# Kernel optimization log

Hardware: AMD Instinct MI355X
Metric: run time of the kernel (lower is better)

Reference implementation:

```python
import jax, jax.numpy as jnp
import numpy as np

HIDDEN = 2048
NH = 32          # num attention heads
NKV = 8          # num key/value heads
HD = HIDDEN // NH  # head_dim = 64
ROPE_BASE = 10000.0
NEG_INF = -1e9


def _rope_interleaved(t, positions):
    # t: [b, s, h, d], interleaved RoPE over full head_dim (flash-attn RotaryEmbedding(interleaved=True))
    d = t.shape[-1]
    inv_freq = 1.0 / (ROPE_BASE ** (jnp.arange(0, d, 2, dtype=jnp.float32) / d))
    ang = positions[:, None].astype(jnp.float32) * inv_freq[None, :]  # [s, d/2]
    cos = jnp.cos(ang)[None, :, None, :]
    sin = jnp.sin(ang)[None, :, None, :]
    t1 = t[..., 0::2]
    t2 = t[..., 1::2]
    out_even = t1 * cos - t2 * sin
    out_odd = t1 * sin + t2 * cos
    return jnp.stack([out_even, out_odd], axis=-1).reshape(t.shape)


def setup_inputs() -> dict:
    key = jax.random.key(0)
    k1, k2, k3 = jax.random.split(key, 3)
    B, S = 2, 2048
    x = jax.random.normal(k1, (B, S, HIDDEN), dtype=jnp.float32)
    mask = jnp.ones((B, S), dtype=jnp.int32)  # padding mask, all valid
    total_head_dim = (NH + 2 * NKV) * HD  # 3072
    scale = 1.0 / np.sqrt(HIDDEN)
    w_qkv = jax.random.normal(k2, (HIDDEN, total_head_dim), dtype=jnp.float32) * scale
    w_o = jax.random.normal(k3, (NH * HD, HIDDEN), dtype=jnp.float32) * scale
    return {"x": x, "mask": mask, "w_qkv": w_qkv, "w_o": w_o}


def reference(x, mask, w_qkv, w_o):
    B, S, _ = x.shape
    kv_size = NKV * HD
    qkv = jnp.einsum('bsh,hd->bsd', x, w_qkv)
    q = qkv[..., :HIDDEN].reshape(B, S, NH, HD)
    kv = qkv[..., HIDDEN:].reshape(B, S, 2, NKV, HD)
    pos = jnp.arange(S)  # seqlen_offset = 0 (input_pos None)
    q = _rope_interleaved(q, pos)
    k = _rope_interleaved(kv[:, :, 0], pos)
    v = kv[:, :, 1]
    # GQA: expand kv heads to NH
    groups = NH // NKV
    k = jnp.repeat(k, groups, axis=2)  # [b, s, NH, HD]
    v = jnp.repeat(v, groups, axis=2)
    scores = jnp.einsum('bqhd,bkhd->bhqk', q, k) / np.sqrt(HD)
    causal = jnp.tril(jnp.ones((S, S), dtype=bool))
    key_valid = mask[:, None, None, :] > 0  # [b,1,1,k]
    scores = jnp.where(causal[None, None] & key_valid, scores, NEG_INF)
    probs = jax.nn.softmax(scores, axis=-1)
    attn = jnp.einsum('bhqk,bkhd->bqhd', probs, v)
    # pad_input writes zeros at padded query positions
    attn = attn * (mask[:, :, None, None] > 0)
    attn = attn.reshape(B, S, NH * HD)
    return jnp.einsum('bsd,dh->bsh', attn, w_o)
```

## Files before the change

kernel.cpp:

```cpp
#include <hip/hip_runtime.h>
#include <hip/hip_bf16.h>
#include <cstdint>
#include <cstddef>

typedef __attribute__((ext_vector_type(8))) short bf16x8;
typedef __attribute__((ext_vector_type(4))) float f32x4;

static constexpr int CB  = 2;
static constexpr int CS  = 2048;
static constexpr int CH  = 2048;
static constexpr int CNH = 32;
static constexpr int CNKV = 8;
static constexpr int CHD = 64;
static constexpr int CTHD = 3072;

__device__ __forceinline__ void gload_lds16(const void* g, void* l) {
  __builtin_amdgcn_global_load_lds(
      (const __attribute__((address_space(1))) unsigned int*)g,
      (__attribute__((address_space(3))) unsigned int*)l, 16, 0, 0);
}

__device__ __forceinline__ unsigned short bfbits(float f) {
  __hip_bfloat16 h = __float2bfloat16(f);
  return *(unsigned short*)&h;
}

__global__ void conv_bf16(const float* __restrict__ in, __hip_bfloat16* __restrict__ out, int n) {
  const int i = (blockIdx.x * 256 + threadIdx.x) * 4;
  if (i >= n) return;
  const float4 v = *(const float4*)(in + i);
  out[i]     = __float2bfloat16(v.x);
  out[i + 1] = __float2bfloat16(v.y);
  out[i + 2] = __float2bfloat16(v.z);
  out[i + 3] = __float2bfloat16(v.w);
}

__global__ __launch_bounds__(256) void transpose_conv(const float* __restrict__ in,
                                                      __hip_bfloat16* __restrict__ out,
                                                      int R, int Cc) {
  __shared__ float t[32][33];
  const int nbx = Cc >> 5;
  const int bx = blockIdx.x % nbx, by = blockIdx.x / nbx;
  const int c0 = bx << 5, r0 = by << 5;
  const int tx = threadIdx.x & 31, ty = threadIdx.x >> 5;
#pragma unroll
  for (int j = 0; j < 32; j += 8)
    t[ty + j][tx] = in[(size_t)(r0 + ty + j) * Cc + c0 + tx];
  __syncthreads();
#pragma unroll
  for (int j = 0; j < 32; j += 8)
    out[(size_t)(c0 + ty + j) * R + r0 + tx] = __float2bfloat16(t[tx][ty + j]);
}

template <typename OutT>
__global__ __launch_bounds__(256) void gemm_bt(const __hip_bfloat16* __restrict__ A,
                                               const __hip_bfloat16* __restrict__ Bt,
                                               OutT* __restrict__ C, int M, int N, int K) {
  __shared__ __hip_bfloat16 As[128 * 32];
  __shared__ __hip_bfloat16 Bs[128 * 32];
  const int tid = threadIdx.x;
  const int lane = tid & 63;
  const int wave = tid >> 6;
  const int nTn = N >> 7;
  const int nwg = gridDim.x;
  const int wg = (blockIdx.x & 7) * (nwg >> 3) + (blockIdx.x >> 3);
  const int tm = wg / nTn, tn = wg % nTn;
  const size_t m0 = (size_t)tm * 128, n0 = (size_t)tn * 128;
  const __hip_bfloat16* Ag = A + m0 * K;
  const __hip_bfloat16* Bg = Bt + n0 * K;
  const int wr = wave >> 1, wc = wave & 1;
  const int rsel = lane & 15, k8 = (lane >> 4) << 3;

  f32x4 acc[4][4];
#pragma unroll
  for (int m = 0; m < 4; ++m)
#pragma unroll
    for (int n = 0; n < 4; ++n) acc[m][n] = (f32x4){0.f, 0.f, 0.f, 0.f};

  for (int k0 = 0; k0 < K; k0 += 32) {
    __syncthreads();
#pragma unroll
    for (int i = 0; i < 2; ++i) {
      const int c = i * 256 + tid;
      const int r = c >> 2, kq = (c & 3) << 3;
      gload_lds16(Ag + (size_t)r * K + k0 + kq, &As[(i * 256 + wave * 64) * 8]);
      gload_lds16(Bg + (size_t)r * K + k0 + kq, &Bs[(i * 256 + wave * 64) * 8]);
    }
    __syncthreads();
    bf16x8 af[4], bfr[4];
#pragma unroll
    for (int m = 0; m < 4; ++m)
      af[m] = *(const bf16x8*)&As[(wr * 64 + m * 16 + rsel) * 32 + k8];
#pragma unroll
    for (int n = 0; n < 4; ++n)
      bfr[n] = *(const bf16x8*)&Bs[(wc * 64 + n * 16 + rsel) * 32 + k8];
#pragma unroll
    for (int m = 0; m < 4; ++m)
#pragma unroll
      for (int n = 0; n < 4; ++n)
        acc[m][n] = __builtin_amdgcn_mfma_f32_16x16x32_bf16(af[m], bfr[n], acc[m][n], 0, 0, 0);
  }

  const int rowb = (lane >> 4) << 2;
#pragma unroll
  for (int m = 0; m < 4; ++m)
#pragma unroll
    for (int n = 0; n < 4; ++n) {
      const size_t r0 = m0 + wr * 64 + m * 16 + rowb;
      const size_t cc = n0 + wc * 64 + n * 16 + rsel;
#pragma unroll
      for (int j = 0; j < 4; ++j) {
        const float v = acc[m][n][j];
        if constexpr (sizeof(OutT) == 4)
          C[(r0 + j) * N + cc] = v;
        else
          C[(r0 + j) * N + cc] = __float2bfloat16(v);
      }
    }
}

__global__ void rope_extract(const __hip_bfloat16* __restrict__ qkv,
                             __hip_bfloat16* __restrict__ Q,
                             __hip_bfloat16* __restrict__ Kr) {
  const int idx = blockIdx.x * 256 + threadIdx.x;
  const int i = idx & 31;
  const int hs = (idx >> 5) % 40;
  const int r = idx / (40 * 32);
  const int srow = r & (CS - 1);
  const int b = r >> 11;
  const float inv = exp2f(-(float)i * (13.287712379549449f / 32.0f));
  const float ang = (float)srow * inv;
  const float sn = sinf(ang), cs = cosf(ang);
  const int col = (hs < CNH) ? hs * CHD + 2 * i : CH + (hs - CNH) * CHD + 2 * i;
  const float t1 = __bfloat162float(qkv[(size_t)r * CTHD + col]);
  const float t2 = __bfloat162float(qkv[(size_t)r * CTHD + col + 1]);
  const float scl = (hs < CNH) ? 0.18033688011112042f : 1.0f;
  const float ev = (t1 * cs - t2 * sn) * scl;
  const float ov = (t1 * sn + t2 * cs) * scl;
  __hip_bfloat16* dst;
  if (hs < CNH)
    dst = Q + ((((size_t)b * CNH + hs) * CS + srow) * CHD + 2 * i);
  else
    dst = Kr + ((((size_t)b * CNKV + (hs - CNH)) * CS + srow) * CHD + 2 * i);
  dst[0] = __float2bfloat16(ev);
  dst[1] = __float2bfloat16(ov);
}

__global__ __launch_bounds__(256) void v_transpose(const __hip_bfloat16* __restrict__ qkv,
                                                   __hip_bfloat16* __restrict__ VT) {
  __shared__ __hip_bfloat16 t[64][72];
  const int bi = blockIdx.x;
  const int stile = bi & 31;
  const int kvh = (bi >> 5) & 7;
  const int b = bi >> 8;
  const int tx = threadIdx.x & 63;
  const int ty = threadIdx.x >> 6;
  const int s0 = stile * 64;
#pragma unroll
  for (int j = 0; j < 16; ++j) {
    const int sl = ty * 16 + j;
    t[sl][tx] = qkv[(size_t)(b * CS + s0 + sl) * CTHD + (CH + CNKV * CHD) + kvh * CHD + tx];
  }
  __syncthreads();
#pragma unroll
  for (int j = 0; j < 16; ++j) {
    const int dl = ty * 16 + j;
    VT[(((size_t)b * CNKV + kvh) * CHD + dl) * CS + s0 + tx] = t[tx][dl];
  }
}

__global__ __launch_bounds__(256) void attn_fa(const __hip_bfloat16* __restrict__ Q,
                                               const __hip_bfloat16* __restrict__ Kr,
                                               const __hip_bfloat16* __restrict__ VT,
                                               const int* __restrict__ mask,
                                               __hip_bfloat16* __restrict__ O) {
  __shared__ __hip_bfloat16 Ks[2][64 * 64];
  __shared__ __hip_bfloat16 Vs[2][64 * 64];
  __shared__ __hip_bfloat16 P4[4][16][72];
  const int kvh = blockIdx.x & 7;
  const int slot = blockIdx.x >> 3;
  const int qw = 127 - (slot >> 1);
  const int b = slot & 1;
  const int tid = threadIdx.x;
  const int wave = tid >> 6, lane = tid & 63;
  const int h = kvh * 4 + wave;
  const int q0 = qw * 16;
  const int rsel = lane & 15;
  const int hi = lane >> 4;
  const int k8 = hi * 8;
  const int rowb = hi * 4;
  const int qr = q0 + rsel;
  const __hip_bfloat16* Qp = Q + (((size_t)b * CNH + h) * CS + q0) * CHD;
  const __hip_bfloat16* Kp = Kr + ((size_t)b * CNKV + kvh) * CS * CHD;
  const __hip_bfloat16* Vp = VT + ((size_t)b * CNKV + kvh) * CHD * CS;
  const int* mp = mask + b * CS;
  __hip_bfloat16(*P)[72] = P4[wave];

  bf16x8 qf[2];
  qf[0] = *(const bf16x8*)(Qp + rsel * CHD + k8);
  qf[1] = *(const bf16x8*)(Qp + rsel * CHD + 32 + k8);

  f32x4 o[4];
#pragma unroll
  for (int nt = 0; nt < 4; ++nt) o[nt] = (f32x4){0.f, 0.f, 0.f, 0.f};
  float mrun = -3e38f, lrun = 0.f;

  const int nkb = (qw >> 2) + 1;

  auto stage = [&](int buf, int key0) {
#pragma unroll
    for (int half = 0; half < 2; ++half) {
      const int c = half * 256 + tid;
      const int r = c >> 3;
      const int swz = ((c & 7) ^ (r & 7)) * 8;
      __hip_bfloat16* kd = &Ks[buf][(half * 256 + wave * 64) * 8];
      __hip_bfloat16* vd = &Vs[buf][(half * 256 + wave * 64) * 8];
      gload_lds16(Kp + (size_t)(key0 + r) * CHD + swz, kd);
      gload_lds16(Vp + (size_t)r * CS + key0 + swz, vd);
    }
  };

  int mcur = mp[lane], mnext = 0;
  stage(0, 0);
  __syncthreads();

  for (int t = 0; t < nkb; ++t) {
    const int cur = t & 1;
    const int key0 = t * 64;
    const bool last = (t == nkb - 1);
    if (!last) {
      stage(cur ^ 1, key0 + 64);
      mnext = mp[key0 + 64 + lane];
    }
    const unsigned long long kvbits = __ballot(mcur > 0);
    const int sz = rsel & 7;
    bf16x8 kc[8];
#pragma unroll
    for (int kt = 0; kt < 4; ++kt) {
      const int row = (kt * 16 + rsel) * 64;
      kc[kt * 2]     = *(const bf16x8*)&Ks[cur][row + ((hi ^ sz) << 3)];
      kc[kt * 2 + 1] = *(const bf16x8*)&Ks[cur][row + (((hi ^ 4) ^ sz) << 3)];
    }
    f32x4 st[4];
#pragma unroll
    for (int kt = 0; kt < 4; ++kt) {
      f32x4 s = (f32x4){0.f, 0.f, 0.f, 0.f};
      s = __builtin_amdgcn_mfma_f32_16x16x32_bf16(kc[kt * 2], qf[0], s, 0, 0, 0);
      s = __builtin_amdgcn_mfma_f32_16x16x32_bf16(kc[kt * 2 + 1], qf[1], s, 0, 0, 0);
      st[kt] = s;
    }
    bf16x8 vf[8];
#pragma unroll
    for (int nt = 0; nt < 4; ++nt) {
      const int row = (nt * 16 + rsel) * 64;
      vf[nt * 2]     = *(const bf16x8*)&Vs[cur][row + ((hi ^ sz) << 3)];
      vf[nt * 2 + 1] = *(const bf16x8*)&Vs[cur][row + (((hi ^ 4) ^ sz) << 3)];
    }
    if (!(kvbits == ~0ull && !last)) {
#pragma unroll
      for (int kt = 0; kt < 4; ++kt)
#pragma unroll
        for (int j = 0; j < 4; ++j) {
          const int idx = kt * 16 + rowb + j;
          const bool bad = !((kvbits >> idx) & 1ull) || (last && key0 + idx > qr);
          if (bad) st[kt][j] = -1e9f;
        }
    }
    float pmax = st[0][0];
#pragma unroll
    for (int kt = 0; kt < 4; ++kt)
#pragma unroll
      for (int j = 0; j < 4; ++j) pmax = fmaxf(pmax, st[kt][j]);
    pmax = fmaxf(pmax, __shfl_xor(pmax, 16));
    pmax = fmaxf(pmax, __shfl_xor(pmax, 32));
    if (__any(pmax > mrun + 8.0f)) {
      const float mn = fmaxf(mrun, pmax);
      const float al = exp2f(mrun - mn);
      mrun = mn;
      lrun *= al;
#pragma unroll
      for (int nt = 0; nt < 4; ++nt)
#pragma unroll
        for (int j = 0; j < 4; ++j) o[nt][j] *= al;
    }
    float ps = 0.f;
#pragma unroll
    for (int kt = 0; kt < 4; ++kt)
#pragma unroll
      for (int j = 0; j < 4; ++j) {
        const float p = exp2f(st[kt][j] - mrun);
        st[kt][j] = p;
        ps += p;
      }
    ps += __shfl_xor(ps, 16);
    ps += __shfl_xor(ps, 32);
    lrun += ps;
#pragma unroll
    for (int kt = 0; kt < 4; ++kt) {
      ushort4 pk;
      pk.x = bfbits(st[kt][0]);
      pk.y = bfbits(st[kt][1]);
      pk.z = bfbits(st[kt][2]);
      pk.w = bfbits(st[kt][3]);
      *(ushort4*)&P[rsel][kt * 16 + rowb] = pk;
    }
    const bf16x8 pb0 = *(const bf16x8*)&P[rsel][k8];
    const bf16x8 pb1 = *(const bf16x8*)&P[rsel][32 + k8];
#pragma unroll
    for (int nt = 0; nt < 4; ++nt) {
      o[nt] = __builtin_amdgcn_mfma_f32_16x16x32_bf16(vf[nt * 2], pb0, o[nt], 0, 0, 0);
      o[nt] = __builtin_amdgcn_mfma_f32_16x16x32_bf16(vf[nt * 2 + 1], pb1, o[nt], 0, 0, 0);
    }
    __syncthreads();
    mcur = mnext;
  }

  const float qm = (mp[qr] > 0) ? 1.0f : 0.0f;
  const float inv = qm / fmaxf(lrun, 1e-20f);
  __hip_bfloat16* Orow = O + (((size_t)b * CS + qr) * CNH + h) * CHD;
#pragma unroll
  for (int nt = 0; nt < 4; ++nt) {
    ushort4 ok;
    ok.x = bfbits(o[nt][0] * inv);
    ok.y = bfbits(o[nt][1] * inv);
    ok.z = bfbits(o[nt][2] * inv);
    ok.w = bfbits(o[nt][3] * inv);
    *(ushort4*)(Orow + nt * 16 + rowb) = ok;
  }
}

extern "C" void kernel_launch(void* const* d_in, const int* in_sizes, int n_in,
                              void* d_out, int out_size, void* d_ws, size_t ws_size,
                              hipStream_t stream) {
  const float* x = (const float*)d_in[0];
  const int* mask = (const int*)d_in[1];
  const float* w_qkv = (const float*)d_in[2];
  const float* w_o = (const float*)d_in[3];
  float* out = (float*)d_out;

  char* ws = (char*)d_ws;
  size_t off = 0;
  auto alloc = [&](size_t bytes) {
    char* p = ws + off;
    off += (bytes + 255) & ~(size_t)255;
    return p;
  };
  const size_t M = (size_t)CB * CS;
  __hip_bfloat16* x_bf  = (__hip_bfloat16*)alloc(M * CH * 2);
  __hip_bfloat16* wqkvT = (__hip_bfloat16*)alloc((size_t)CTHD * CH * 2);
  __hip_bfloat16* woT   = (__hip_bfloat16*)alloc((size_t)CH * CH * 2);
  __hip_bfloat16* qkv   = (__hip_bfloat16*)alloc(M * CTHD * 2);
  __hip_bfloat16* Qb    = (__hip_bfloat16*)alloc((size_t)CB * CNH * CS * CHD * 2);
  __hip_bfloat16* Kb    = (__hip_bfloat16*)alloc((size_t)CB * CNKV * CS * CHD * 2);
  __hip_bfloat16* VTb   = (__hip_bfloat16*)alloc((size_t)CB * CNKV * CHD * CS * 2);
  __hip_bfloat16* attnb = (__hip_bfloat16*)alloc(M * CH * 2);

  conv_bf16<<<(int)(M * CH / 4 / 256), 256, 0, stream>>>(x, x_bf, (int)(M * CH));
  transpose_conv<<<(CTHD / 32) * (CH / 32), 256, 0, stream>>>(w_qkv, wqkvT, CH, CTHD);
  transpose_conv<<<(CH / 32) * (CH / 32), 256, 0, stream>>>(w_o, woT, CH, CH);
  gemm_bt<__hip_bfloat16><<<(int)(M / 128) * (CTHD / 128), 256, 0, stream>>>(
      x_bf, wqkvT, qkv, (int)M, CTHD, CH);
  rope_extract<<<(int)(M * 40 * 32 / 256), 256, 0, stream>>>(qkv, Qb, Kb);
  v_transpose<<<CB * CNKV * 32, 256, 0, stream>>>(qkv, VTb);
  attn_fa<<<CB * CNKV * 128, 256, 0, stream>>>(Qb, Kb, VTb, mask, attnb);
  gemm_bt<float><<<(int)(M / 128) * (CH / 128), 256, 0, stream>>>(
      attnb, woT, out, (int)M, CH, CH);
}
```

Baseline: 247.0 us.

## Process two 16-row query sub-tiles per wave in flash attention

```diff
diff --git a/kernel.cpp b/kernel.cpp
--- a/kernel.cpp
+++ b/kernel.cpp
@@ -176,36 +176,39 @@
                                                __hip_bfloat16* __restrict__ O) {
   __shared__ __hip_bfloat16 Ks[2][64 * 64];
   __shared__ __hip_bfloat16 Vs[2][64 * 64];
-  __shared__ __hip_bfloat16 P4[4][16][72];
+  __shared__ __hip_bfloat16 P4[4][2][16][72];
   const int kvh = blockIdx.x & 7;
   const int slot = blockIdx.x >> 3;
-  const int qw = 127 - (slot >> 1);
+  const int qw = 63 - (slot >> 1);
   const int b = slot & 1;
   const int tid = threadIdx.x;
   const int wave = tid >> 6, lane = tid & 63;
   const int h = kvh * 4 + wave;
-  const int q0 = qw * 16;
+  const int q0 = qw * 32;
   const int rsel = lane & 15;
   const int hi = lane >> 4;
   const int k8 = hi * 8;
   const int rowb = hi * 4;
-  const int qr = q0 + rsel;
   const __hip_bfloat16* Qp = Q + (((size_t)b * CNH + h) * CS + q0) * CHD;
   const __hip_bfloat16* Kp = Kr + ((size_t)b * CNKV + kvh) * CS * CHD;
   const __hip_bfloat16* Vp = VT + ((size_t)b * CNKV + kvh) * CHD * CS;
   const int* mp = mask + b * CS;
-  __hip_bfloat16(*P)[72] = P4[wave];
-
-  bf16x8 qf[2];
-  qf[0] = *(const bf16x8*)(Qp + rsel * CHD + k8);
-  qf[1] = *(const bf16x8*)(Qp + rsel * CHD + 32 + k8);
-
-  f32x4 o[4];
-#pragma unroll
-  for (int nt = 0; nt < 4; ++nt) o[nt] = (f32x4){0.f, 0.f, 0.f, 0.f};
-  float mrun = -3e38f, lrun = 0.f;
-
-  const int nkb = (qw >> 2) + 1;
+
+  bf16x8 qf[2][2];
+#pragma unroll
+  for (int s = 0; s < 2; ++s) {
+    qf[s][0] = *(const bf16x8*)(Qp + (s * 16 + rsel) * CHD + k8);
+    qf[s][1] = *(const bf16x8*)(Qp + (s * 16 + rsel) * CHD + 32 + k8);
+  }
+
+  f32x4 o[2][4];
+#pragma unroll
+  for (int s = 0; s < 2; ++s)
+#pragma unroll
+    for (int nt = 0; nt < 4; ++nt) o[s][nt] = (f32x4){0.f, 0.f, 0.f, 0.f};
+  float mrun[2] = {-3e38f, -3e38f}, lrun[2] = {0.f, 0.f};
+
+  const int nkb = (qw >> 1) + 1;
 
   auto stage = [&](int buf, int key0) {
 #pragma unroll
@@ -241,14 +244,75 @@
       kc[kt * 2]     = *(const bf16x8*)&Ks[cur][row + ((hi ^ sz) << 3)];
       kc[kt * 2 + 1] = *(const bf16x8*)&Ks[cur][row + (((hi ^ 4) ^ sz) << 3)];
     }
-    f32x4 st[4];
+    f32x4 st[2][4];
 #pragma unroll
     for (int kt = 0; kt < 4; ++kt) {
-      f32x4 s = (f32x4){0.f, 0.f, 0.f, 0.f};
-      s = __builtin_amdgcn_mfma_f32_16x16x32_bf16(kc[kt * 2], qf[0], s, 0, 0, 0);
-      s = __builtin_amdgcn_mfma_f32_16x16x32_bf16(kc[kt * 2 + 1], qf[1], s, 0, 0, 0);
-      st[kt] = s;
-    }
+#pragma unroll
+      for (int s = 0; s < 2; ++s) {
+        f32x4 acc = (f32x4){0.f, 0.f, 0.f, 0.f};
+        acc = __builtin_amdgcn_mfma_f32_16x16x32_bf16(kc[kt * 2], qf[s][0], acc, 0, 0, 0);
+        acc = __builtin_amdgcn_mfma_f32_16x16x32_bf16(kc[kt * 2 + 1], qf[s][1], acc, 0, 0, 0);
+        st[s][kt] = acc;
+      }
+    }
+#pragma unroll
+    for (int s = 0; s < 2; ++s) {
+      const int qs = q0 + s * 16;
+      const int qr = qs + rsel;
+      if (kvbits != ~0ull || key0 + 63 > qs) {
+#pragma unroll
+        for (int kt = 0; kt < 4; ++kt)
+#pragma unroll
+          for (int j = 0; j < 4; ++j) {
+            const int idx = kt * 16 + rowb + j;
+            const bool bad = !((kvbits >> idx) & 1ull) || (key0 + idx > qr);
+            if (bad) st[s][kt][j] = -1e9f;
+          }
+      }
+    }
+#pragma unroll
+    for (int s = 0; s < 2; ++s) {
+      float pmax = st[s][0][0];
+#pragma unroll
+      for (int kt = 0; kt < 4; ++kt)
+#pragma unroll
+        for (int j = 0; j < 4; ++j) pmax = fmaxf(pmax, st[s][kt][j]);
+      pmax = fmaxf(pmax, __shfl_xor(pmax, 16));
+      pmax = fmaxf(pmax, __shfl_xor(pmax, 32));
+      if (__any(pmax > mrun[s] + 8.0f)) {
+        const float mn = fmaxf(mrun[s], pmax);
+        const float al = exp2f(mrun[s] - mn);
+        mrun[s] = mn;
+        lrun[s] *= al;
+#pragma unroll
+        for (int nt = 0; nt < 4; ++nt)
+#pragma unroll
+          for (int j = 0; j < 4; ++j) o[s][nt][j] *= al;
+      }
+      float ps = 0.f;
+#pragma unroll
+      for (int kt = 0; kt < 4; ++kt)
+#pragma unroll
+        for (int j = 0; j < 4; ++j) {
+          const float p = exp2f(st[s][kt][j] - mrun[s]);
+          st[s][kt][j] = p;
+          ps += p;
+        }
+      ps += __shfl_xor(ps, 16);
+      ps += __shfl_xor(ps, 32);
+      lrun[s] += ps;
+    }
+#pragma unroll
+    for (int s = 0; s < 2; ++s)
+#pragma unroll
+      for (int kt = 0; kt < 4; ++kt) {
+        ushort4 pk;
+        pk.x = bfbits(st[s][kt][0]);
+        pk.y = bfbits(st[s][kt][1]);
+        pk.z = bfbits(st[s][kt][2]);
+        pk.w = bfbits(st[s][kt][3]);
+        *(ushort4*)&P4[wave][s][rsel][kt * 16 + rowb] = pk;
+      }
     bf16x8 vf[8];
 #pragma unroll
     for (int nt = 0; nt < 4; ++nt) {
@@ -256,76 +320,38 @@
       vf[nt * 2]     = *(const bf16x8*)&Vs[cur][row + ((hi ^ sz) << 3)];
       vf[nt * 2 + 1] = *(const bf16x8*)&Vs[cur][row + (((hi ^ 4) ^ sz) << 3)];
     }
-    if (!(kvbits == ~0ull && !last)) {
-#pragma unroll
-      for (int kt = 0; kt < 4; ++kt)
-#pragma unroll
-        for (int j = 0; j < 4; ++j) {
-          const int idx = kt * 16 + rowb + j;
-          const bool bad = !((kvbits >> idx) & 1ull) || (last && key0 + idx > qr);
-          if (bad) st[kt][j] = -1e9f;
-        }
-    }
-    float pmax = st[0][0];
-#pragma unroll
-    for (int kt = 0; kt < 4; ++kt)
-#pragma unroll
-      for (int j = 0; j < 4; ++j) pmax = fmaxf(pmax, st[kt][j]);
-    pmax = fmaxf(pmax, __shfl_xor(pmax, 16));
-    pmax = fmaxf(pmax, __shfl_xor(pmax, 32));
-    if (__any(pmax > mrun + 8.0f)) {
-      const float mn = fmaxf(mrun, pmax);
-      const float al = exp2f(mrun - mn);
-      mrun = mn;
-      lrun *= al;
-#pragma unroll
-      for (int nt = 0; nt < 4; ++nt)
-#pragma unroll
-        for (int j = 0; j < 4; ++j) o[nt][j] *= al;
-    }
-    float ps = 0.f;
-#pragma unroll
-    for (int kt = 0; kt < 4; ++kt)
-#pragma unroll
-      for (int j = 0; j < 4; ++j) {
-        const float p = exp2f(st[kt][j] - mrun);
-        st[kt][j] = p;
-        ps += p;
-      }
-    ps += __shfl_xor(ps, 16);
-    ps += __shfl_xor(ps, 32);
-    lrun += ps;
-#pragma unroll
-    for (int kt = 0; kt < 4; ++kt) {
-      ushort4 pk;
-      pk.x = bfbits(st[kt][0]);
-      pk.y = bfbits(st[kt][1]);
-      pk.z = bfbits(st[kt][2]);
-      pk.w = bfbits(st[kt][3]);
-      *(ushort4*)&P[rsel][kt * 16 + rowb] = pk;
-    }
-    const bf16x8 pb0 = *(const bf16x8*)&P[rsel][k8];
-    const bf16x8 pb1 = *(const bf16x8*)&P[rsel][32 + k8];
-#pragma unroll
-    for (int nt = 0; nt < 4; ++nt) {
-      o[nt] = __builtin_amdgcn_mfma_f32_16x16x32_bf16(vf[nt * 2], pb0, o[nt], 0, 0, 0);
-      o[nt] = __builtin_amdgcn_mfma_f32_16x16x32_bf16(vf[nt * 2 + 1], pb1, o[nt], 0, 0, 0);
-    }
+    bf16x8 pb[2][2];
+#pragma unroll
+    for (int s = 0; s < 2; ++s) {
+      pb[s][0] = *(const bf16x8*)&P4[wave][s][rsel][k8];
+      pb[s][1] = *(const bf16x8*)&P4[wave][s][rsel][32 + k8];
+    }
+#pragma unroll
+    for (int nt = 0; nt < 4; ++nt)
+#pragma unroll
+      for (int s = 0; s < 2; ++s) {
+        o[s][nt] = __builtin_amdgcn_mfma_f32_16x16x32_bf16(vf[nt * 2], pb[s][0], o[s][nt], 0, 0, 0);
+        o[s][nt] = __builtin_amdgcn_mfma_f32_16x16x32_bf16(vf[nt * 2 + 1], pb[s][1], o[s][nt], 0, 0, 0);
+      }
     __syncthreads();
     mcur = mnext;
   }
 
-  const float qm = (mp[qr] > 0) ? 1.0f : 0.0f;
-  const float inv = qm / fmaxf(lrun, 1e-20f);
-  __hip_bfloat16* Orow = O + (((size_t)b * CS + qr) * CNH + h) * CHD;
-#pragma unroll
-  for (int nt = 0; nt < 4; ++nt) {
-    ushort4 ok;
-    ok.x = bfbits(o[nt][0] * inv);
-    ok.y = bfbits(o[nt][1] * inv);
-    ok.z = bfbits(o[nt][2] * inv);
-    ok.w = bfbits(o[nt][3] * inv);
-    *(ushort4*)(Orow + nt * 16 + rowb) = ok;
+#pragma unroll
+  for (int s = 0; s < 2; ++s) {
+    const int qr = q0 + s * 16 + rsel;
+    const float qm = (mp[qr] > 0) ? 1.0f : 0.0f;
+    const float inv = qm / fmaxf(lrun[s], 1e-20f);
+    __hip_bfloat16* Orow = O + (((size_t)b * CS + qr) * CNH + h) * CHD;
+#pragma unroll
+    for (int nt = 0; nt < 4; ++nt) {
+      ushort4 ok;
+      ok.x = bfbits(o[s][nt][0] * inv);
+      ok.y = bfbits(o[s][nt][1] * inv);
+      ok.z = bfbits(o[s][nt][2] * inv);
+      ok.w = bfbits(o[s][nt][3] * inv);
+      *(ushort4*)(Orow + nt * 16 + rowb) = ok;
+    }
   }
 }
 
@@ -362,7 +388,7 @@
       x_bf, wqkvT, qkv, (int)M, CTHD, CH);
   rope_extract<<<(int)(M * 40 * 32 / 256), 256, 0, stream>>>(qkv, Qb, Kb);
   v_transpose<<<CB * CNKV * 32, 256, 0, stream>>>(qkv, VTb);
-  attn_fa<<<CB * CNKV * 128, 256, 0, stream>>>(Qb, Kb, VTb, mask, attnb);
+  attn_fa<<<CB * CNKV * 64, 256, 0, stream>>>(Qb, Kb, VTb, mask, attnb);
   gemm_bt<float><<<(int)(M / 128) * (CH / 128), 256, 0, stream>>>(
       attnb, woT, out, (int)M, CH, CH);
 }
```

New measurement: 293.3 us. +18.7%, slower.

## Fuse RoPE, Q/K scatter and V transpose into QKV GEMM epilogue

Applied to the files above, without the earlier changes.

```diff
diff --git a/kernel.cpp b/kernel.cpp
--- a/kernel.cpp
+++ b/kernel.cpp
@@ -33,6 +33,14 @@
   out[i + 1] = __float2bfloat16(v.y);
   out[i + 2] = __float2bfloat16(v.z);
   out[i + 3] = __float2bfloat16(v.w);
+}
+
+__global__ void trig_table(float2* __restrict__ tab) {
+  const int idx = blockIdx.x * 256 + threadIdx.x;
+  const int s = idx >> 5, i = idx & 31;
+  const float inv = exp2f(-(float)i * (13.287712379549449f / 32.0f));
+  const float ang = (float)s * inv;
+  tab[idx] = make_float2(cosf(ang), sinf(ang));
 }
 
 __global__ __launch_bounds__(256) void transpose_conv(const float* __restrict__ in,
@@ -119,54 +127,105 @@
     }
 }
 
-__global__ void rope_extract(const __hip_bfloat16* __restrict__ qkv,
-                             __hip_bfloat16* __restrict__ Q,
-                             __hip_bfloat16* __restrict__ Kr) {
-  const int idx = blockIdx.x * 256 + threadIdx.x;
-  const int i = idx & 31;
-  const int hs = (idx >> 5) % 40;
-  const int r = idx / (40 * 32);
-  const int srow = r & (CS - 1);
-  const int b = r >> 11;
-  const float inv = exp2f(-(float)i * (13.287712379549449f / 32.0f));
-  const float ang = (float)srow * inv;
-  const float sn = sinf(ang), cs = cosf(ang);
-  const int col = (hs < CNH) ? hs * CHD + 2 * i : CH + (hs - CNH) * CHD + 2 * i;
-  const float t1 = __bfloat162float(qkv[(size_t)r * CTHD + col]);
-  const float t2 = __bfloat162float(qkv[(size_t)r * CTHD + col + 1]);
-  const float scl = (hs < CNH) ? 0.18033688011112042f : 1.0f;
-  const float ev = (t1 * cs - t2 * sn) * scl;
-  const float ov = (t1 * sn + t2 * cs) * scl;
-  __hip_bfloat16* dst;
-  if (hs < CNH)
-    dst = Q + ((((size_t)b * CNH + hs) * CS + srow) * CHD + 2 * i);
-  else
-    dst = Kr + ((((size_t)b * CNKV + (hs - CNH)) * CS + srow) * CHD + 2 * i);
-  dst[0] = __float2bfloat16(ev);
-  dst[1] = __float2bfloat16(ov);
-}
-
-__global__ __launch_bounds__(256) void v_transpose(const __hip_bfloat16* __restrict__ qkv,
-                                                   __hip_bfloat16* __restrict__ VT) {
-  __shared__ __hip_bfloat16 t[64][72];
-  const int bi = blockIdx.x;
-  const int stile = bi & 31;
-  const int kvh = (bi >> 5) & 7;
-  const int b = bi >> 8;
-  const int tx = threadIdx.x & 63;
-  const int ty = threadIdx.x >> 6;
-  const int s0 = stile * 64;
-#pragma unroll
-  for (int j = 0; j < 16; ++j) {
-    const int sl = ty * 16 + j;
-    t[sl][tx] = qkv[(size_t)(b * CS + s0 + sl) * CTHD + (CH + CNKV * CHD) + kvh * CHD + tx];
+__global__ __launch_bounds__(256) void gemm_qkv(const __hip_bfloat16* __restrict__ A,
+                                                const __hip_bfloat16* __restrict__ Bt,
+                                                const float2* __restrict__ tab,
+                                                __hip_bfloat16* __restrict__ Qb,
+                                                __hip_bfloat16* __restrict__ Kb,
+                                                __hip_bfloat16* __restrict__ VTb) {
+  constexpr int M = CB * CS, N = CTHD, K = CH;
+  __shared__ __hip_bfloat16 As[128 * 32];
+  __shared__ __hip_bfloat16 Bs[128 * 32];
+  const int tid = threadIdx.x;
+  const int lane = tid & 63;
+  const int wave = tid >> 6;
+  const int nTn = N >> 7;
+  const int nwg = gridDim.x;
+  const int wg = (blockIdx.x & 7) * (nwg >> 3) + (blockIdx.x >> 3);
+  const int tm = wg / nTn, tn = wg % nTn;
+  const int m0 = tm * 128, n0 = tn * 128;
+  const __hip_bfloat16* Ag = A + (size_t)m0 * K;
+  const __hip_bfloat16* Bg = Bt + (size_t)n0 * K;
+  const int wr = wave >> 1, wc = wave & 1;
+  const int rsel = lane & 15, k8 = (lane >> 4) << 3;
+
+  f32x4 acc[4][4];
+#pragma unroll
+  for (int m = 0; m < 4; ++m)
+#pragma unroll
+    for (int n = 0; n < 4; ++n) acc[m][n] = (f32x4){0.f, 0.f, 0.f, 0.f};
+
+  for (int k0 = 0; k0 < K; k0 += 32) {
+    __syncthreads();
+#pragma unroll
+    for (int i = 0; i < 2; ++i) {
+      const int c = i * 256 + tid;
+      const int r = c >> 2, kq = (c & 3) << 3;
+      gload_lds16(Ag + (size_t)r * K + k0 + kq, &As[(i * 256 + wave * 64) * 8]);
+      gload_lds16(Bg + (size_t)r * K + k0 + kq, &Bs[(i * 256 + wave * 64) * 8]);
+    }
+    __syncthreads();
+    bf16x8 af[4], bfr[4];
+#pragma unroll
+    for (int m = 0; m < 4; ++m)
+      af[m] = *(const bf16x8*)&As[(wr * 64 + m * 16 + rsel) * 32 + k8];
+#pragma unroll
+    for (int n = 0; n < 4; ++n)
+      bfr[n] = *(const bf16x8*)&Bs[(wc * 64 + n * 16 + rsel) * 32 + k8];
+#pragma unroll
+    for (int m = 0; m < 4; ++m)
+#pragma unroll
+      for (int n = 0; n < 4; ++n)
+        acc[m][n] = __builtin_amdgcn_mfma_f32_16x16x32_bf16(af[m], bfr[n], acc[m][n], 0, 0, 0);
   }
-  __syncthreads();
-#pragma unroll
-  for (int j = 0; j < 16; ++j) {
-    const int dl = ty * 16 + j;
-    VT[(((size_t)b * CNKV + kvh) * CHD + dl) * CS + s0 + tx] = t[tx][dl];
-  }
+
+  const int rowb = (lane >> 4) << 2;
+  const float sgn = (rsel & 1) ? 1.0f : -1.0f;
+#pragma unroll
+  for (int m = 0; m < 4; ++m)
+#pragma unroll
+    for (int n = 0; n < 4; ++n) {
+      const int rowg = m0 + wr * 64 + m * 16 + rowb;
+      const int cc0 = n0 + wc * 64 + n * 16;
+      const int ccl = cc0 + rsel;
+      const int bb = rowg >> 11;
+      if (cc0 < CH) {
+        const int hh = ccl >> 6, d = ccl & 63, ii = (d >> 1) & 31;
+        __hip_bfloat16* base = Qb + (((size_t)bb * CNH + hh) * CS) * CHD + d;
+#pragma unroll
+        for (int j = 0; j < 4; ++j) {
+          const int s = (rowg + j) & (CS - 1);
+          const float x = acc[m][n][j];
+          const float y = __shfl_xor(x, 1);
+          const float2 cs_ = tab[s * 32 + ii];
+          const float v = (x * cs_.x + sgn * y * cs_.y) * 0.18033688011112042f;
+          base[(size_t)s * CHD] = __float2bfloat16(v);
+        }
+      } else if (cc0 < CH + CNKV * CHD) {
+        const int ckl = ccl - CH;
+        const int kvh = ckl >> 6, d = ckl & 63, ii = (d >> 1) & 31;
+        __hip_bfloat16* base = Kb + (((size_t)bb * CNKV + kvh) * CS) * CHD + d;
+#pragma unroll
+        for (int j = 0; j < 4; ++j) {
+          const int s = (rowg + j) & (CS - 1);
+          const float x = acc[m][n][j];
+          const float y = __shfl_xor(x, 1);
+          const float2 cs_ = tab[s * 32 + ii];
+          const float v = x * cs_.x + sgn * y * cs_.y;
+          base[(size_t)s * CHD] = __float2bfloat16(v);
+        }
+      } else {
+        const int cvl = ccl - (CH + CNKV * CHD);
+        const int kvh = cvl >> 6, d = cvl & 63;
+        const int s0 = rowg & (CS - 1);
+        ushort4 ok;
+        ok.x = bfbits(acc[m][n][0]);
+        ok.y = bfbits(acc[m][n][1]);
+        ok.z = bfbits(acc[m][n][2]);
+        ok.w = bfbits(acc[m][n][3]);
+        *(ushort4*)(VTb + (((size_t)bb * CNKV + kvh) * CHD + d) * CS + s0) = ok;
+      }
+    }
 }
 
 __global__ __launch_bounds__(256) void attn_fa(const __hip_bfloat16* __restrict__ Q,
@@ -349,7 +408,7 @@
   __hip_bfloat16* x_bf  = (__hip_bfloat16*)alloc(M * CH * 2);
   __hip_bfloat16* wqkvT = (__hip_bfloat16*)alloc((size_t)CTHD * CH * 2);
   __hip_bfloat16* woT   = (__hip_bfloat16*)alloc((size_t)CH * CH * 2);
-  __hip_bfloat16* qkv   = (__hip_bfloat16*)alloc(M * CTHD * 2);
+  float2*         tab   = (float2*)alloc((size_t)CS * 32 * sizeof(float2));
   __hip_bfloat16* Qb    = (__hip_bfloat16*)alloc((size_t)CB * CNH * CS * CHD * 2);
   __hip_bfloat16* Kb    = (__hip_bfloat16*)alloc((size_t)CB * CNKV * CS * CHD * 2);
   __hip_bfloat16* VTb   = (__hip_bfloat16*)alloc((size_t)CB * CNKV * CHD * CS * 2);
@@ -358,10 +417,9 @@
   conv_bf16<<<(int)(M * CH / 4 / 256), 256, 0, stream>>>(x, x_bf, (int)(M * CH));
   transpose_conv<<<(CTHD / 32) * (CH / 32), 256, 0, stream>>>(w_qkv, wqkvT, CH, CTHD);
   transpose_conv<<<(CH / 32) * (CH / 32), 256, 0, stream>>>(w_o, woT, CH, CH);
-  gemm_bt<__hip_bfloat16><<<(int)(M / 128) * (CTHD / 128), 256, 0, stream>>>(
-      x_bf, wqkvT, qkv, (int)M, CTHD, CH);
-  rope_extract<<<(int)(M * 40 * 32 / 256), 256, 0, stream>>>(qkv, Qb, Kb);
-  v_transpose<<<CB * CNKV * 32, 256, 0, stream>>>(qkv, VTb);
+  trig_table<<<(CS * 32) / 256, 256, 0, stream>>>(tab);
+  gemm_qkv<<<(int)(M / 128) * (CTHD / 128), 256, 0, stream>>>(
+      x_bf, wqkvT, tab, Qb, Kb, VTb);
   attn_fa<<<CB * CNKV * 128, 256, 0, stream>>>(Qb, Kb, VTb, mask, attnb);
   gemm_bt<float><<<(int)(M / 128) * (CH / 128), 256, 0, stream>>>(
       attnb, woT, out, (int)M, CH, CH);
```

Result: slower. 256.5 us (+3.9%).

## Replace 128x128 GEMM with double-buffered 256x256 tile GEMM using swizzled LDS

Applied to the files above, without the earlier changes.

```diff
diff --git a/kernel.cpp b/kernel.cpp
--- a/kernel.cpp
+++ b/kernel.cpp
@@ -53,64 +53,93 @@
 }
 
 template <typename OutT>
-__global__ __launch_bounds__(256) void gemm_bt(const __hip_bfloat16* __restrict__ A,
+__global__ __launch_bounds__(512) void gemm256(const __hip_bfloat16* __restrict__ A,
                                                const __hip_bfloat16* __restrict__ Bt,
                                                OutT* __restrict__ C, int M, int N, int K) {
-  __shared__ __hip_bfloat16 As[128 * 32];
-  __shared__ __hip_bfloat16 Bs[128 * 32];
+  __shared__ __hip_bfloat16 As[2][256 * 64];
+  __shared__ __hip_bfloat16 Bs[2][256 * 64];
   const int tid = threadIdx.x;
   const int lane = tid & 63;
   const int wave = tid >> 6;
-  const int nTn = N >> 7;
+  const int nTn = N >> 8;
   const int nwg = gridDim.x;
   const int wg = (blockIdx.x & 7) * (nwg >> 3) + (blockIdx.x >> 3);
   const int tm = wg / nTn, tn = wg % nTn;
-  const size_t m0 = (size_t)tm * 128, n0 = (size_t)tn * 128;
+  const size_t m0 = (size_t)tm * 256, n0 = (size_t)tn * 256;
   const __hip_bfloat16* Ag = A + m0 * K;
   const __hip_bfloat16* Bg = Bt + n0 * K;
-  const int wr = wave >> 1, wc = wave & 1;
-  const int rsel = lane & 15, k8 = (lane >> 4) << 3;
-
-  f32x4 acc[4][4];
-#pragma unroll
-  for (int m = 0; m < 4; ++m)
-#pragma unroll
-    for (int n = 0; n < 4; ++n) acc[m][n] = (f32x4){0.f, 0.f, 0.f, 0.f};
-
-  for (int k0 = 0; k0 < K; k0 += 32) {
-    __syncthreads();
-#pragma unroll
-    for (int i = 0; i < 2; ++i) {
-      const int c = i * 256 + tid;
-      const int r = c >> 2, kq = (c & 3) << 3;
-      gload_lds16(Ag + (size_t)r * K + k0 + kq, &As[(i * 256 + wave * 64) * 8]);
-      gload_lds16(Bg + (size_t)r * K + k0 + kq, &Bs[(i * 256 + wave * 64) * 8]);
-    }
-    __syncthreads();
-    bf16x8 af[4], bfr[4];
-#pragma unroll
-    for (int m = 0; m < 4; ++m)
-      af[m] = *(const bf16x8*)&As[(wr * 64 + m * 16 + rsel) * 32 + k8];
-#pragma unroll
-    for (int n = 0; n < 4; ++n)
-      bfr[n] = *(const bf16x8*)&Bs[(wc * 64 + n * 16 + rsel) * 32 + k8];
-#pragma unroll
-    for (int m = 0; m < 4; ++m)
-#pragma unroll
-      for (int n = 0; n < 4; ++n)
-        acc[m][n] = __builtin_amdgcn_mfma_f32_16x16x32_bf16(af[m], bfr[n], acc[m][n], 0, 0, 0);
-  }
-
-  const int rowb = (lane >> 4) << 2;
-#pragma unroll
-  for (int m = 0; m < 4; ++m)
-#pragma unroll
-    for (int n = 0; n < 4; ++n) {
-      const size_t r0 = m0 + wr * 64 + m * 16 + rowb;
-      const size_t cc = n0 + wc * 64 + n * 16 + rsel;
+  const int wr = wave >> 2, wc = wave & 3;
+  const int rsel = lane & 15, hi = lane >> 4;
+  const int szr = rsel & 7;
+
+  f32x4 acc[8][4];
+#pragma unroll
+  for (int mf = 0; mf < 8; ++mf)
+#pragma unroll
+    for (int nf = 0; nf < 4; ++nf) acc[mf][nf] = (f32x4){0.f, 0.f, 0.f, 0.f};
+
+  auto stage = [&](int buf, int k0) {
+#pragma unroll
+    for (int i = 0; i < 4; ++i) {
+      const int c = i * 512 + tid;
+      const int r = c >> 3;
+      const int swz = ((c & 7) ^ (r & 7)) << 3;
+      gload_lds16(Ag + (size_t)r * K + k0 + swz, &As[buf][(i * 512 + wave * 64) * 8]);
+      gload_lds16(Bg + (size_t)r * K + k0 + swz, &Bs[buf][(i * 512 + wave * 64) * 8]);
+    }
+  };
+
+  const int nt = K >> 6;
+  stage(0, 0);
+  asm volatile("s_waitcnt vmcnt(0)" ::: "memory");
+  __builtin_amdgcn_sched_barrier(0);
+  __builtin_amdgcn_s_barrier();
+
+  for (int t = 0; t < nt; ++t) {
+    const int cur = t & 1;
+    if (t + 1 < nt) {
+      stage(cur ^ 1, (t + 1) << 6);
+      asm volatile("s_waitcnt vmcnt(8)" ::: "memory");
+    } else {
+      asm volatile("s_waitcnt vmcnt(0)" ::: "memory");
+    }
+    __builtin_amdgcn_sched_barrier(0);
+    __builtin_amdgcn_s_barrier();
+
+#pragma unroll
+    for (int kk = 0; kk < 2; ++kk) {
+      bf16x8 af[8], bf[4];
+#pragma unroll
+      for (int mf = 0; mf < 8; ++mf) {
+        const int row = wr * 128 + mf * 16 + rsel;
+        af[mf] = *(const bf16x8*)&As[cur][row * 64 + ((((kk << 2) | hi) ^ szr) << 3)];
+      }
+#pragma unroll
+      for (int nf = 0; nf < 4; ++nf) {
+        const int row = wc * 64 + nf * 16 + rsel;
+        bf[nf] = *(const bf16x8*)&Bs[cur][row * 64 + ((((kk << 2) | hi) ^ szr) << 3)];
+      }
+#pragma unroll
+      for (int mf = 0; mf < 8; ++mf)
+#pragma unroll
+        for (int nf = 0; nf < 4; ++nf)
+          acc[mf][nf] = __builtin_amdgcn_mfma_f32_16x16x32_bf16(af[mf], bf[nf], acc[mf][nf], 0, 0, 0);
+    }
+    asm volatile("s_waitcnt lgkmcnt(0)" ::: "memory");
+    __builtin_amdgcn_sched_barrier(0);
+    __builtin_amdgcn_s_barrier();
+  }
+
+  const int rowb = hi << 2;
+#pragma unroll
+  for (int mf = 0; mf < 8; ++mf)
+#pragma unroll
+    for (int nf = 0; nf < 4; ++nf) {
+      const size_t r0 = m0 + wr * 128 + mf * 16 + rowb;
+      const size_t cc = n0 + wc * 64 + nf * 16 + rsel;
 #pragma unroll
       for (int j = 0; j < 4; ++j) {
-        const float v = acc[m][n][j];
+        const float v = acc[mf][nf][j];
         if constexpr (sizeof(OutT) == 4)
           C[(r0 + j) * N + cc] = v;
         else
@@ -358,11 +387,11 @@
   conv_bf16<<<(int)(M * CH / 4 / 256), 256, 0, stream>>>(x, x_bf, (int)(M * CH));
   transpose_conv<<<(CTHD / 32) * (CH / 32), 256, 0, stream>>>(w_qkv, wqkvT, CH, CTHD);
   transpose_conv<<<(CH / 32) * (CH / 32), 256, 0, stream>>>(w_o, woT, CH, CH);
-  gemm_bt<__hip_bfloat16><<<(int)(M / 128) * (CTHD / 128), 256, 0, stream>>>(
+  gemm256<__hip_bfloat16><<<(int)(M / 256) * (CTHD / 256), 512, 0, stream>>>(
       x_bf, wqkvT, qkv, (int)M, CTHD, CH);
   rope_extract<<<(int)(M * 40 * 32 / 256), 256, 0, stream>>>(qkv, Qb, Kb);
   v_transpose<<<CB * CNKV * 32, 256, 0, stream>>>(qkv, VTb);
   attn_fa<<<CB * CNKV * 128, 256, 0, stream>>>(Qb, Kb, VTb, mask, attnb);
-  gemm_bt<float><<<(int)(M / 128) * (CH / 128), 256, 0, stream>>>(
+  gemm256<float><<<(int)(M / 256) * (CH / 256), 512, 0, stream>>>(
       attnb, woT, out, (int)M, CH, CH);
 }
```

New measurement: 254.4 us. 1.03x slower.
